# Kernel optimization log

Measured on AMD Instinct MI355X. Metric: run time of the kernel, lower is better.

Reference implementation:

```python
import jax, jax.numpy as jnp
import numpy as np

NONLIN = jnp.tanh  # configurable gate/candidate nonlinearity ('nonlin' init arg)

T, B, I, H = 1024, 64, 256, 512


def setup_inputs() -> dict:
    key = jax.random.key(0)
    k1, k2, k3 = jax.random.split(key, 3)
    s_i = 1.0 / np.sqrt(I)
    s_h = 1.0 / np.sqrt(H)
    return {
        "x": jax.random.normal(k1, (T, B, I), dtype=jnp.float32),
        "Wi": jax.random.normal(k2, (I, 4 * H), dtype=jnp.float32) * s_i,
        "Wh": jax.random.normal(k3, (H, 4 * H), dtype=jnp.float32) * s_h,
        "bi": jnp.zeros((4 * H,), dtype=jnp.float32),
        "bh": jnp.zeros((4 * H,), dtype=jnp.float32),
        "h0": jnp.zeros((B, H), dtype=jnp.float32),
        "c0": jnp.zeros((B, H), dtype=jnp.float32),
    }


def reference(x, Wi, Wh, bi, bh, h0, c0):
    # Precompute input projection for all timesteps in one big GEMM: [T,B,4H]
    x_proj = jnp.einsum('tbi,ig->tbg', x, Wi) + bi

    def step(carry, xp_t):
        h, c = carry
        gates = xp_t + h @ Wh + bh            # [B, 4H]
        i_g, f_g, g_g, o_g = jnp.split(gates, 4, axis=-1)
        i_g = jax.nn.sigmoid(i_g)
        f_g = jax.nn.sigmoid(f_g)
        o_g = jax.nn.sigmoid(o_g)
        g_g = NONLIN(g_g)
        c_new = f_g * c + i_g * g_g
        h_new = o_g * NONLIN(c_new)
        return (h_new, c_new), h_new

    (h_T, c_T), hs = jax.lax.scan(step, (h0, c0), x_proj)
    return hs  # [T, B, H] hidden states for every timestep
```

## Files before the change

### kernel.cpp

```cpp
#include <hip/hip_runtime.h>
#include <math.h>


#define TT      1024
#define BB      64
#define II      256
#define HH      512
#define G4H     2048
#define RPB     16
#define NRG     4
#define NCG     32
#define THREADS 1024

typedef short  bf16x8 __attribute__((ext_vector_type(8)));
typedef float  f32x4  __attribute__((ext_vector_type(4)));

__device__ __forceinline__ unsigned int cvtpk_bf16(float a, float b) {
    unsigned int r;
    asm volatile("v_cvt_pk_bf16_f32 %0, %1, %2" : "=v"(r) : "v"(a), "v"(b));
    return r;
}
__device__ __forceinline__ void coh_store_u(unsigned int* p, unsigned int v) {
    asm volatile("global_store_dword %0, %1, off sc0 sc1"
                 :: "v"(p), "v"(v) : "memory");
}
__device__ __forceinline__ float fast_tanh(float v) {
    const float e = __expf(-2.0f * fabsf(v));
    const float r = (1.0f - e) / (1.0f + e);
    return v < 0.0f ? -r : r;
}
__device__ __forceinline__ float sigm(float v) {
    return 1.0f / (1.0f + __expf(-v));
}

__device__ __forceinline__ void cvt_frag(float4 v0, float4 v1,
                                         uint4& hi, uint4& lo) {
    hi.x = cvtpk_bf16(v0.x, v0.y);
    hi.y = cvtpk_bf16(v0.z, v0.w);
    hi.z = cvtpk_bf16(v1.x, v1.y);
    hi.w = cvtpk_bf16(v1.z, v1.w);
    lo.x = cvtpk_bf16(v0.x - __uint_as_float(hi.x << 16),
                      v0.y - __uint_as_float(hi.x & 0xffff0000u));
    lo.y = cvtpk_bf16(v0.z - __uint_as_float(hi.y << 16),
                      v0.w - __uint_as_float(hi.y & 0xffff0000u));
    lo.z = cvtpk_bf16(v1.x - __uint_as_float(hi.z << 16),
                      v1.y - __uint_as_float(hi.z & 0xffff0000u));
    lo.w = cvtpk_bf16(v1.z - __uint_as_float(hi.w << 16),
                      v1.w - __uint_as_float(hi.w & 0xffff0000u));
}

__device__ __forceinline__ void unpack8(uint4 a, uint4 b,
                                        uint4& fh, uint4& fl) {
    fh.x = (a.x >> 16) | (a.y & 0xffff0000u);
    fh.y = (a.z >> 16) | (a.w & 0xffff0000u);
    fh.z = (b.x >> 16) | (b.y & 0xffff0000u);
    fh.w = (b.z >> 16) | (b.w & 0xffff0000u);
    fl.x = (a.x & 0xffffu) | (a.y << 16);
    fl.y = (a.z & 0xffffu) | (a.w << 16);
    fl.z = (b.x & 0xffffu) | (b.y << 16);
    fl.w = (b.z & 0xffffu) | (b.w << 16);
}

__global__ void init_ctr(unsigned int* c) { c[threadIdx.x] = 0; }

__global__ __launch_bounds__(THREADS) void lstm_persist(
    const float* __restrict__ x,
    const float* __restrict__ Wi,
    const float* __restrict__ Wh,
    const float* __restrict__ bi,
    const float* __restrict__ bh,
    const float* __restrict__ h0p,
    const float* __restrict__ c0p,
    float* __restrict__ out,
    unsigned int* __restrict__ hpk,
    unsigned int* __restrict__ ctr)
{
    const int tid   = threadIdx.x;
    const int cg    = blockIdx.x & 31;
    const int rg    = blockIdx.x >> 5;
    const int row0  = rg * RPB;
    const int cell0 = cg * 16;
    const int wv    = tid >> 6;
    const int lane  = tid & 63;
    const int n4    = wv >> 2;
    const int k4    = wv & 3;

    __shared__ uint4 aFH[24 * 64];
    __shared__ uint4 aFL[24 * 64];
    __shared__ float red[16 * 64 * 4];
    __shared__ float c_lds[RPB][16];

    const int s_ls = tid & 63;
    const int s_r  = s_ls & 15;
    const int s_k2 = ((s_ls >> 4) & 3) * 8;
    const int xkk  = tid >> 6;
    const int hkc  = (tid >> 6) * 32 + s_k2;

    bf16x8 wH[6], wL[6];
    {
        const int J = n4 * HH + cell0 + (lane & 15);
        #pragma unroll
        for (int s = 0; s < 6; ++s) {
            const int kk = (s < 2) ? (k4 * 2 + s) : (8 + k4 * 4 + (s - 2));
            const int kb = kk * 32 + (lane >> 4) * 8;
            float w[8];
            #pragma unroll
            for (int e = 0; e < 8; ++e) {
                const int k = kb + e;
                w[e] = (k < II) ? Wi[(size_t)k * G4H + J]
                                : Wh[(size_t)(k - II) * G4H + J];
            }
            uint4 hi, lo;
            cvt_frag(make_float4(w[0], w[1], w[2], w[3]),
                     make_float4(w[4], w[5], w[6], w[7]), hi, lo);
            wH[s] = *(bf16x8*)&hi;
            wL[s] = *(bf16x8*)&lo;
        }
    }

    float b4[4];
    if (tid < 256) {
        const int r = tid >> 4, m = tid & 15;
        #pragma unroll
        for (int g = 0; g < 4; ++g)
            b4[g] = bi[g * HH + cell0 + m] + bh[g * HH + cell0 + m];
        c_lds[r][m] = c0p[(size_t)(row0 + r) * HH + cell0 + m];
    }

    if (tid < 512) {
        const float* xr = x + (size_t)(row0 + s_r) * II + xkk * 32 + s_k2;
        uint4 hi, lo;
        cvt_frag(*(const float4*)xr, *(const float4*)(xr + 4), hi, lo);
        aFH[tid] = hi; aFL[tid] = lo;
    }
    {
        const float* hr = h0p + (size_t)(row0 + s_r) * HH + hkc;
        uint4 hi, lo;
        cvt_frag(*(const float4*)hr, *(const float4*)(hr + 4), hi, lo);
        aFH[512 + tid] = hi; aFL[512 + tid] = lo;
    }
    __syncthreads();

    f32x4 acc = {0.f, 0.f, 0.f, 0.f};
    #pragma unroll
    for (int q = 0; q < 2; ++q) {
        const int kk = k4 * 2 + q;
        const bf16x8 ah = *(const bf16x8*)&aFH[kk * 64 + lane];
        const bf16x8 al = *(const bf16x8*)&aFL[kk * 64 + lane];
        acc = __builtin_amdgcn_mfma_f32_16x16x32_bf16(ah, wH[q], acc, 0, 0, 0);
        acc = __builtin_amdgcn_mfma_f32_16x16x32_bf16(ah, wL[q], acc, 0, 0, 0);
        acc = __builtin_amdgcn_mfma_f32_16x16x32_bf16(al, wH[q], acc, 0, 0, 0);
    }

    unsigned int* myctr = ctr + rg * 32;

    for (int t = 0; t < TT; ++t) {
        const bool more = (t + 1 < TT);

        float4 xv0, xv1;
        if (more && tid < 512) {
            const float* xr = x + ((size_t)(t + 1) * BB + row0 + s_r) * II
                              + xkk * 32 + s_k2;
            xv0 = *(const float4*)xr;
            xv1 = *(const float4*)(xr + 4);
        }

        #pragma unroll
        for (int q = 0; q < 4; ++q) {
            const int kk = 8 + k4 * 4 + q;
            const bf16x8 ah = *(const bf16x8*)&aFH[kk * 64 + lane];
            const bf16x8 al = *(const bf16x8*)&aFL[kk * 64 + lane];
            acc = __builtin_amdgcn_mfma_f32_16x16x32_bf16(ah, wH[2 + q], acc, 0, 0, 0);
            acc = __builtin_amdgcn_mfma_f32_16x16x32_bf16(ah, wL[2 + q], acc, 0, 0, 0);
            acc = __builtin_amdgcn_mfma_f32_16x16x32_bf16(al, wH[2 + q], acc, 0, 0, 0);
        }

        ((f32x4*)red)[wv * 64 + lane] = acc;
        if (more && tid < 512) {
            uint4 hi, lo;
            cvt_frag(xv0, xv1, hi, lo);
            aFH[tid] = hi; aFL[tid] = lo;
        }
        __syncthreads();

        if (more && wv >= 4) {
            acc = (f32x4){0.f, 0.f, 0.f, 0.f};
            #pragma unroll
            for (int q = 0; q < 2; ++q) {
                const int kk = k4 * 2 + q;
                const bf16x8 ah = *(const bf16x8*)&aFH[kk * 64 + lane];
                const bf16x8 al = *(const bf16x8*)&aFL[kk * 64 + lane];
                acc = __builtin_amdgcn_mfma_f32_16x16x32_bf16(ah, wH[q], acc, 0, 0, 0);
                acc = __builtin_amdgcn_mfma_f32_16x16x32_bf16(ah, wL[q], acc, 0, 0, 0);
                acc = __builtin_amdgcn_mfma_f32_16x16x32_bf16(al, wH[q], acc, 0, 0, 0);
            }
        }

        if (tid < 256) {
            const int r = tid >> 4, m = tid & 15;
            const int lc  = m + 16 * (r >> 2);
            const int reg = r & 3;
            float g4[4];
            #pragma unroll
            for (int g = 0; g < 4; ++g) {
                float s = b4[g];
                #pragma unroll
                for (int p = 0; p < 4; ++p)
                    s += red[((g * 4 + p) * 64 + lc) * 4 + reg];
                g4[g] = s;
            }
            const float ig = sigm(g4[0]);
            const float fg = sigm(g4[1]);
            const float gg = fast_tanh(g4[2]);
            const float og = sigm(g4[3]);
            const float cn = fg * c_lds[r][m] + ig * gg;
            c_lds[r][m] = cn;
            const float hv = og * fast_tanh(cn);
            out[((size_t)t * BB + row0 + r) * HH + cell0 + m] = hv;
            if (more) {
                const unsigned int hb = cvtpk_bf16(hv, hv) & 0xffffu;
                const float hf = __uint_as_float(hb << 16);
                const unsigned int lb = cvtpk_bf16(hv - hf, hv - hf) & 0xffffu;
                coh_store_u(&hpk[((size_t)(t & 1) * BB + row0 + r) * HH
                                 + cell0 + m], (hb << 16) | lb);
            }
        }

        if (wv < 4) asm volatile("s_waitcnt vmcnt(0) lgkmcnt(0)" ::: "memory");
        __syncthreads();
        if (more) {
            if (tid == 0)
                __hip_atomic_fetch_add(myctr, 1u, __ATOMIC_RELAXED,
                                       __HIP_MEMORY_SCOPE_AGENT);

            if (wv < 4) {
                acc = (f32x4){0.f, 0.f, 0.f, 0.f};
                #pragma unroll
                for (int q = 0; q < 2; ++q) {
                    const int kk = k4 * 2 + q;
                    const bf16x8 ah = *(const bf16x8*)&aFH[kk * 64 + lane];
                    const bf16x8 al = *(const bf16x8*)&aFL[kk * 64 + lane];
                    acc = __builtin_amdgcn_mfma_f32_16x16x32_bf16(ah, wH[q], acc, 0, 0, 0);
                    acc = __builtin_amdgcn_mfma_f32_16x16x32_bf16(ah, wL[q], acc, 0, 0, 0);
                    acc = __builtin_amdgcn_mfma_f32_16x16x32_bf16(al, wH[q], acc, 0, 0, 0);
                }
            }

            if (tid == 0) {
                const unsigned int target = 32u * (unsigned int)(t + 1);
                while (__hip_atomic_load(myctr, __ATOMIC_RELAXED,
                                         __HIP_MEMORY_SCOPE_AGENT) < target) {
                    __builtin_amdgcn_s_sleep(1);
                }
            }
            __syncthreads();

            const unsigned int* hb = hpk + ((size_t)(t & 1) * BB + row0 + s_r) * HH + hkc;
            uint4 q0, q1;
            asm volatile(
                "global_load_dwordx4 %0, %2, off sc0 sc1\n\t"
                "global_load_dwordx4 %1, %2, off offset:16 sc0 sc1\n\t"
                "s_waitcnt vmcnt(0)"
                : "=&v"(q0), "=&v"(q1)
                : "v"(hb)
                : "memory");

            {
                uint4 fh, fl;
                unpack8(q0, q1, fh, fl);
                aFH[512 + tid] = fh; aFL[512 + tid] = fl;
            }
            __syncthreads();
        }
    }
}

extern "C" void kernel_launch(void* const* d_in, const int* in_sizes, int n_in,
                              void* d_out, int out_size, void* d_ws, size_t ws_size,
                              hipStream_t stream) {
    const float* x  = (const float*)d_in[0];
    const float* Wi = (const float*)d_in[1];
    const float* Wh = (const float*)d_in[2];
    const float* bi = (const float*)d_in[3];
    const float* bh = (const float*)d_in[4];
    const float* h0 = (const float*)d_in[5];
    const float* c0 = (const float*)d_in[6];
    float* out = (float*)d_out;

    unsigned int* hpk = (unsigned int*)d_ws;
    unsigned int* ctr = (unsigned int*)((char*)d_ws + 2 * BB * HH * 4);

    init_ctr<<<1, 128, 0, stream>>>(ctr);

    void* args[] = { (void*)&x, (void*)&Wi, (void*)&Wh, (void*)&bi,
                     (void*)&bh, (void*)&h0, (void*)&c0, (void*)&out,
                     (void*)&hpk, (void*)&ctr };
    hipError_t e = hipLaunchCooperativeKernel((const void*)lstm_persist,
                                              dim3(NRG * NCG), dim3(THREADS),
                                              args, 0, stream);
    if (e != hipSuccess) {
        (void)hipGetLastError();
        lstm_persist<<<dim3(NRG * NCG), dim3(THREADS), 0, stream>>>(
            x, Wi, Wh, bi, bh, h0, c0, out, hpk, ctr);
    }
}
```

Baseline: 4.052 ms.

## Tag hidden-state stores with step and speculatively prefetch h before barrier wait

Each exchanged hidden value is now stored as an 8-byte pair holding the packed bf16 hi/lo value and a step tag. Consumers issue relaxed atomic loads of the next h fragment before waiting on the inter-block counter, then check the tags after the barrier and reload only when any tag is stale. This is meant to hide the global-load latency of the h exchange behind the recurrent MFMA work and the spin wait. The MFMA work split between wave halves is also unified so that all waves run after the counter increment. In exchange, exchange traffic doubles, and the counter barrier is still kept, so the gain is limited to overlapping load latency.

```diff
diff --git a/kernel.cpp b/kernel.cpp
--- a/kernel.cpp
+++ b/kernel.cpp
@@ -20,8 +20,8 @@
     asm volatile("v_cvt_pk_bf16_f32 %0, %1, %2" : "=v"(r) : "v"(a), "v"(b));
     return r;
 }
-__device__ __forceinline__ void coh_store_u(unsigned int* p, unsigned int v) {
-    asm volatile("global_store_dword %0, %1, off sc0 sc1"
+__device__ __forceinline__ void coh_store_u2(uint2* p, uint2 v) {
+    asm volatile("global_store_dwordx2 %0, %1, off sc0 sc1"
                  :: "v"(p), "v"(v) : "memory");
 }
 __device__ __forceinline__ float fast_tanh(float v) {
@@ -72,7 +72,7 @@
     const float* __restrict__ h0p,
     const float* __restrict__ c0p,
     float* __restrict__ out,
-    unsigned int* __restrict__ hpk,
+    uint2* __restrict__ hx,
     unsigned int* __restrict__ ctr)
 {
     const int tid   = threadIdx.x;
@@ -183,19 +183,6 @@
         }
         __syncthreads();
 
-        if (more && wv >= 4) {
-            acc = (f32x4){0.f, 0.f, 0.f, 0.f};
-            #pragma unroll
-            for (int q = 0; q < 2; ++q) {
-                const int kk = k4 * 2 + q;
-                const bf16x8 ah = *(const bf16x8*)&aFH[kk * 64 + lane];
-                const bf16x8 al = *(const bf16x8*)&aFL[kk * 64 + lane];
-                acc = __builtin_amdgcn_mfma_f32_16x16x32_bf16(ah, wH[q], acc, 0, 0, 0);
-                acc = __builtin_amdgcn_mfma_f32_16x16x32_bf16(ah, wL[q], acc, 0, 0, 0);
-                acc = __builtin_amdgcn_mfma_f32_16x16x32_bf16(al, wH[q], acc, 0, 0, 0);
-            }
-        }
-
         if (tid < 256) {
             const int r = tid >> 4, m = tid & 15;
             const int lc  = m + 16 * (r >> 2);
@@ -218,11 +205,14 @@
             const float hv = og * fast_tanh(cn);
             out[((size_t)t * BB + row0 + r) * HH + cell0 + m] = hv;
             if (more) {
-                const unsigned int hb = cvtpk_bf16(hv, hv) & 0xffffu;
-                const float hf = __uint_as_float(hb << 16);
-                const unsigned int lb = cvtpk_bf16(hv - hf, hv - hf) & 0xffffu;
-                coh_store_u(&hpk[((size_t)(t & 1) * BB + row0 + r) * HH
-                                 + cell0 + m], (hb << 16) | lb);
+                const unsigned int hb16 = cvtpk_bf16(hv, hv) & 0xffffu;
+                const float hf = __uint_as_float(hb16 << 16);
+                const unsigned int lb16 = cvtpk_bf16(hv - hf, hv - hf) & 0xffffu;
+                uint2 pr;
+                pr.x = (hb16 << 16) | lb16;
+                pr.y = (unsigned int)(t + 1);
+                coh_store_u2(&hx[((size_t)(t & 1) * BB + row0 + r) * HH
+                                 + cell0 + m], pr);
             }
         }
 
@@ -233,21 +223,33 @@
                 __hip_atomic_fetch_add(myctr, 1u, __ATOMIC_RELAXED,
                                        __HIP_MEMORY_SCOPE_AGENT);
 
-            if (wv < 4) {
-                acc = (f32x4){0.f, 0.f, 0.f, 0.f};
-                #pragma unroll
-                for (int q = 0; q < 2; ++q) {
-                    const int kk = k4 * 2 + q;
-                    const bf16x8 ah = *(const bf16x8*)&aFH[kk * 64 + lane];
-                    const bf16x8 al = *(const bf16x8*)&aFL[kk * 64 + lane];
-                    acc = __builtin_amdgcn_mfma_f32_16x16x32_bf16(ah, wH[q], acc, 0, 0, 0);
-                    acc = __builtin_amdgcn_mfma_f32_16x16x32_bf16(ah, wL[q], acc, 0, 0, 0);
-                    acc = __builtin_amdgcn_mfma_f32_16x16x32_bf16(al, wH[q], acc, 0, 0, 0);
-                }
-            }
+            const unsigned long long* hb8 = (const unsigned long long*)
+                (hx + ((size_t)(t & 1) * BB + row0 + s_r) * HH + hkc);
+            unsigned long long g[8];
+            #pragma unroll
+            for (int i = 0; i < 8; ++i)
+                g[i] = __hip_atomic_load(hb8 + i, __ATOMIC_RELAXED,
+                                         __HIP_MEMORY_SCOPE_AGENT);
+
+            acc = (f32x4){0.f, 0.f, 0.f, 0.f};
+            #pragma unroll
+            for (int q = 0; q < 2; ++q) {
+                const int kk = k4 * 2 + q;
+                const bf16x8 ah = *(const bf16x8*)&aFH[kk * 64 + lane];
+                const bf16x8 al = *(const bf16x8*)&aFL[kk * 64 + lane];
+                acc = __builtin_amdgcn_mfma_f32_16x16x32_bf16(ah, wH[q], acc, 0, 0, 0);
+                acc = __builtin_amdgcn_mfma_f32_16x16x32_bf16(ah, wL[q], acc, 0, 0, 0);
+                acc = __builtin_amdgcn_mfma_f32_16x16x32_bf16(al, wH[q], acc, 0, 0, 0);
+            }
+
+            const unsigned int tgt = (unsigned int)(t + 1);
+            bool ok = true;
+            #pragma unroll
+            for (int i = 0; i < 8; ++i)
+                ok &= ((unsigned int)(g[i] >> 32) == tgt);
 
             if (tid == 0) {
-                const unsigned int target = 32u * (unsigned int)(t + 1);
+                const unsigned int target = 32u * tgt;
                 while (__hip_atomic_load(myctr, __ATOMIC_RELAXED,
                                          __HIP_MEMORY_SCOPE_AGENT) < target) {
                     __builtin_amdgcn_s_sleep(1);
@@ -255,19 +257,30 @@
             }
             __syncthreads();
 
-            const unsigned int* hb = hpk + ((size_t)(t & 1) * BB + row0 + s_r) * HH + hkc;
-            uint4 q0, q1;
-            asm volatile(
-                "global_load_dwordx4 %0, %2, off sc0 sc1\n\t"
-                "global_load_dwordx4 %1, %2, off offset:16 sc0 sc1\n\t"
-                "s_waitcnt vmcnt(0)"
-                : "=&v"(q0), "=&v"(q1)
-                : "v"(hb)
-                : "memory");
+            unsigned int v0 = (unsigned int)g[0], v1 = (unsigned int)g[1],
+                         v2 = (unsigned int)g[2], v3 = (unsigned int)g[3],
+                         v4 = (unsigned int)g[4], v5 = (unsigned int)g[5],
+                         v6 = (unsigned int)g[6], v7 = (unsigned int)g[7];
+            if (!ok) {
+                uint4 r0, r1, r2, r3;
+                asm volatile(
+                    "global_load_dwordx4 %0, %4, off sc0 sc1\n\t"
+                    "global_load_dwordx4 %1, %4, off offset:16 sc0 sc1\n\t"
+                    "global_load_dwordx4 %2, %4, off offset:32 sc0 sc1\n\t"
+                    "global_load_dwordx4 %3, %4, off offset:48 sc0 sc1\n\t"
+                    "s_waitcnt vmcnt(0)"
+                    : "=&v"(r0), "=&v"(r1), "=&v"(r2), "=&v"(r3)
+                    : "v"(hb8)
+                    : "memory");
+                v0 = r0.x; v1 = r0.z; v2 = r1.x; v3 = r1.z;
+                v4 = r2.x; v5 = r2.z; v6 = r3.x; v7 = r3.z;
+            }
 
             {
+                uint4 a4 = {v0, v1, v2, v3};
+                uint4 b4v = {v4, v5, v6, v7};
                 uint4 fh, fl;
-                unpack8(q0, q1, fh, fl);
+                unpack8(a4, b4v, fh, fl);
                 aFH[512 + tid] = fh; aFL[512 + tid] = fl;
             }
             __syncthreads();
@@ -287,20 +300,20 @@
     const float* c0 = (const float*)d_in[6];
     float* out = (float*)d_out;
 
-    unsigned int* hpk = (unsigned int*)d_ws;
-    unsigned int* ctr = (unsigned int*)((char*)d_ws + 2 * BB * HH * 4);
+    uint2* hx = (uint2*)d_ws;
+    unsigned int* ctr = (unsigned int*)((char*)d_ws + 2 * BB * HH * 8);
 
     init_ctr<<<1, 128, 0, stream>>>(ctr);
 
     void* args[] = { (void*)&x, (void*)&Wi, (void*)&Wh, (void*)&bi,
                      (void*)&bh, (void*)&h0, (void*)&c0, (void*)&out,
-                     (void*)&hpk, (void*)&ctr };
+                     (void*)&hx, (void*)&ctr };
     hipError_t e = hipLaunchCooperativeKernel((const void*)lstm_persist,
                                               dim3(NRG * NCG), dim3(THREADS),
                                               args, 0, stream);
     if (e != hipSuccess) {
         (void)hipGetLastError();
         lstm_persist<<<dim3(NRG * NCG), dim3(THREADS), 0, stream>>>(
-            x, Wi, Wh, bi, bh, h0, c0, out, hpk, ctr);
-    }
-}
+            x, Wi, Wh, bi, bh, h0, c0, out, hx, ctr);
+    }
+}
```

Result: slower. 6.236 ms (+53.9%).
